# Optimization experiments

Hardware: AMD Instinct MI355X
Metric: run time of the kernel (lower is better)

Reference implementation:

```python
import jax, jax.numpy as jnp
import numpy as np


def setup_inputs() -> dict:
    key = jax.random.key(0)
    ks = jax.random.split(key, 7)
    C, Cq = 128, 16  # channels, channels//8
    B, H, W = 8, 64, 64
    s = 0.05
    return {
        "x": jax.random.normal(ks[0], (B, C, H, W), jnp.float32),
        "wq": jax.random.normal(ks[1], (Cq, C), jnp.float32) * s,
        "bq": jnp.zeros((Cq,), jnp.float32),
        "wk": jax.random.normal(ks[2], (Cq, C), jnp.float32) * s,
        "bk": jnp.zeros((Cq,), jnp.float32),
        "wv": jax.random.normal(ks[3], (C, C), jnp.float32) * s,
        "bv": jnp.zeros((C,), jnp.float32),
    }


def reference(x, wq, bq, wk, bk, wv, bv):
    B, C, H, W = x.shape
    N = H * W
    dk = wq.shape[0]  # channels // 8
    xf = x.reshape(B, C, N)  # [B, C, N]
    # 1x1 convs == per-pixel linear maps over channels
    q = jnp.einsum('oc,bcn->bon', wq, xf) + bq[None, :, None]  # [B, dk, N]
    k = jnp.einsum('oc,bcn->bon', wk, xf) + bk[None, :, None]  # [B, dk, N]
    v = jnp.einsum('oc,bcn->bon', wv, xf) + bv[None, :, None]  # [B, C, N]
    # scores[b,i,j] = <q[:,i], k[:,j]> / sqrt(dk)
    scores = jnp.einsum('bdi,bdj->bij', q, k) / jnp.sqrt(jnp.asarray(dk, x.dtype))
    attn = jax.nn.softmax(scores, axis=-1)  # softmax over key dim j
    # out[b,c,i] = sum_j v[b,c,j] * attn[b,i,j]
    out = jnp.einsum('bcj,bij->bci', v, attn)
    return out.reshape(B, C, H, W) + x
```

## Files before the change

kernel.cpp:

```cpp
#include <hip/hip_runtime.h>
#include <hip/hip_bf16.h>

#define BATCH 8
#define CDIM  128
#define DK    16
#define NPIX  4096
#define VSTR  72

typedef __attribute__((ext_vector_type(4)))  float    f32x4;
typedef __attribute__((ext_vector_type(16))) float    f32x16;
typedef __attribute__((ext_vector_type(8)))  short    s16x8;
typedef __attribute__((ext_vector_type(4)))  unsigned u32x4;

__device__ __forceinline__ short f2bf(float f) {
    union { float fv; unsigned u; } un; un.fv = f;
    unsigned r = un.u + 0x7FFFu + ((un.u >> 16) & 1u);
    return (short)(r >> 16);
}
__device__ __forceinline__ float bf2f(short s) {
    union { unsigned u; float f; } un; un.u = ((unsigned)(unsigned short)s) << 16;
    return un.f;
}
__device__ __forceinline__ float fexp2(float x) {
#if __has_builtin(__builtin_amdgcn_exp2f)
    return __builtin_amdgcn_exp2f(x);
#else
    return exp2f(x);
#endif
}
__device__ __forceinline__ unsigned pkbf(float lo, float hi) {
    __hip_bfloat162 h = __float22bfloat162_rn(make_float2(lo, hi));
    return *reinterpret_cast<unsigned*>(&h);
}
__device__ __forceinline__ f32x16 zero16() {
    f32x16 z;
    #pragma unroll
    for (int i = 0; i < 16; ++i) z[i] = 0.f;
    return z;
}

#define C2F 0.36067376022224085f
#define WPFRAGS (10 * 4 * 64)

__global__ __launch_bounds__(256) void wprep(
    const float* __restrict__ wq, const float* __restrict__ wk,
    const float* __restrict__ wv, short* __restrict__ Wp)
{
    const int mt   = blockIdx.x;
    const int t    = threadIdx.x;
    const int kt   = t >> 6;
    const int lane = t & 63;
    const int m    = mt * 16 + (lane & 15);
    const int c0   = kt * 32 + ((lane >> 4) << 3);

    const float* src; float scl = 1.f;
    if (m < 16)      { src = wq + m * CDIM; scl = C2F; }
    else if (m < 32) { src = wk + (m - 16) * CDIM; }
    else             { src = wv + (m - 32) * CDIM; }

    s16x8 frag;
    #pragma unroll
    for (int i = 0; i < 8; ++i) frag[i] = f2bf(src[c0 + i] * scl);
    *(s16x8*)(Wp + (((size_t)(mt * 4 + kt) * 64 + lane) << 3)) = frag;
}

__global__ __launch_bounds__(256) void qkv_proj(
    const float* __restrict__ x, const short* __restrict__ Wp,
    const float* __restrict__ bq, const float* __restrict__ bk,
    const float* __restrict__ bv,
    short* __restrict__ Qt, short* __restrict__ Kt, short* __restrict__ Vb)
{
    const int tid   = threadIdx.x;
    const int bid   = blockIdx.x;
    const int b     = bid >> 6;
    const int nbase = (bid & 63) << 6;

    const int lane = tid & 63;
    const int lo   = lane & 15;
    const int hi   = lane >> 4;
    const int n    = ((tid >> 6) << 4) + lo;
    const int ng   = nbase + n;

    const float* xb = x + (((size_t)(b * CDIM)) << 12) + ng;

    s16x8 bfr[4];
    #pragma unroll
    for (int kt = 0; kt < 4; ++kt) {
        const float* xp = xb + (((size_t)(kt * 32 + hi * 8)) << 12);
        float v0 = xp[0];
        float v1 = xp[(size_t)1 << 12];
        float v2 = xp[(size_t)2 << 12];
        float v3 = xp[(size_t)3 << 12];
        float v4 = xp[(size_t)4 << 12];
        float v5 = xp[(size_t)5 << 12];
        float v6 = xp[(size_t)6 << 12];
        float v7 = xp[(size_t)7 << 12];
        union { u32x4 u; s16x8 v; } pk;
        pk.u[0] = pkbf(v0, v1); pk.u[1] = pkbf(v2, v3);
        pk.u[2] = pkbf(v4, v5); pk.u[3] = pkbf(v6, v7);
        bfr[kt] = pk.v;
    }

    f32x4 acc[10];
    #pragma unroll
    for (int mt = 0; mt < 10; ++mt) { acc[mt][0]=0.f; acc[mt][1]=0.f; acc[mt][2]=0.f; acc[mt][3]=0.f; }

    #pragma unroll
    for (int kt = 0; kt < 4; ++kt) {
        #pragma unroll
        for (int mt = 0; mt < 10; ++mt) {
            const s16x8 af = *(const s16x8*)(Wp + (((size_t)(mt * 4 + kt) * 64 + lane) << 3));
            acc[mt] = __builtin_amdgcn_mfma_f32_16x16x32_bf16(af, bfr[kt], acc[mt], 0, 0, 0);
        }
    }

    const int m4 = hi << 2;
    {
        uint2 pk;
        pk.x = pkbf(acc[0][0] + bq[m4 + 0] * C2F, acc[0][1] + bq[m4 + 1] * C2F);
        pk.y = pkbf(acc[0][2] + bq[m4 + 2] * C2F, acc[0][3] + bq[m4 + 3] * C2F);
        *(uint2*)(Qt + ((((size_t)(b << 12)) + ng) << 4) + m4) = pk;
    }
    {
        uint2 pk;
        pk.x = pkbf(acc[1][0] + bk[m4 + 0], acc[1][1] + bk[m4 + 1]);
        pk.y = pkbf(acc[1][2] + bk[m4 + 2], acc[1][3] + bk[m4 + 3]);
        *(uint2*)(Kt + ((((size_t)(b << 12)) + ng) << 4) + m4) = pk;
    }
    #pragma unroll
    for (int mt = 2; mt < 10; ++mt) {
        #pragma unroll
        for (int r = 0; r < 4; ++r) {
            const int c = (mt - 2) * 16 + m4 + r;
            Vb[(((size_t)(b * CDIM + c)) << 12) + ng] = f2bf(acc[mt][r] + bv[c]);
        }
    }
}

template<int KSPLIT, bool DIRECT>
__global__ __launch_bounds__(256, 3) void attn_part(
    const short* __restrict__ Qt, const short* __restrict__ Kt,
    const short* __restrict__ Vb, const float* __restrict__ x,
    float* __restrict__ out, short* __restrict__ Op, float* __restrict__ lsum)
{
    constexpr int NKEY = NPIX / KSPLIT;
    constexpr int NT   = NKEY / 64;
    __shared__ __align__(16) short vs[2][CDIM * VSTR];

    const int tid = threadIdx.x;
    const int bid = blockIdx.x;
    const int qb  = bid & 31;
    const int kc  = (bid >> 5) % KSPLIT;
    const int b   = bid / (32 * KSPLIT);
    const int q0  = qb * 128 + (tid >> 6) * 32;
    const int l31 = tid & 31;
    const int hi2 = (tid >> 5) & 1;
    const int kq  = hi2 << 3;
    const int pi  = (l31 & ~12) | ((l31 & 4) << 1) | ((l31 & 8) >> 1);

    const s16x8 qB = *(const s16x8*)(Qt + (((size_t)(b << 12) + q0 + l31) << 4) + kq);

    const int j8  = tid & 7;
    const int cb8 = tid >> 3;
    const short* vsrc = Vb + (((size_t)(b * CDIM + cb8)) << 12) + (j8 << 3);
    const int vdoff = cb8 * VSTR + (j8 << 3);
    const size_t cstr = (size_t)32 << 12;

    const int jbase0 = kc * NKEY;
    const short* ktb = Kt + ((size_t)(b << 12) << 4);

    f32x16 O0 = zero16(), O1 = zero16(), O2 = zero16(), O3 = zero16();
    float l_acc = 0.f;

    s16x8 r0, r1, r2, r3;
    #define VLOAD(jb) do {                                   \
        r0 = *(const s16x8*)(vsrc + (jb));                   \
        r1 = *(const s16x8*)(vsrc + (jb) + cstr);            \
        r2 = *(const s16x8*)(vsrc + (jb) + 2 * cstr);        \
        r3 = *(const s16x8*)(vsrc + (jb) + 3 * cstr);        \
    } while (0)
    #define VSTORE(bufi) do {                                \
        short* vd_ = &vs[bufi][vdoff];                       \
        *(s16x8*)(vd_)             = r0;                     \
        *(s16x8*)(vd_ + 32 * VSTR) = r1;                     \
        *(s16x8*)(vd_ + 64 * VSTR) = r2;                     \
        *(s16x8*)(vd_ + 96 * VSTR) = r3;                     \
    } while (0)
    #define KLOAD(jb) (*(const s16x8*)(ktb + (((size_t)((jb) + pi)) << 4) + kq))
    #define LDSV(vb_, ct, ch) (*(const s16x8*)((vb_) + ((ct) * 32 + l31) * VSTR + ((ch) << 3)))

    #define LOADVF(dst, h, vb_) do {                         \
        const int ch_ = ((h) << 1) | hi2;                    \
        dst[0] = LDSV(vb_, 0, ch_);                          \
        dst[1] = LDSV(vb_, 1, ch_);                          \
        dst[2] = LDSV(vb_, 2, ch_);                          \
        dst[3] = LDSV(vb_, 3, ch_);                          \
    } while (0)

    #define HALFP(sv, ktl, vf) do {                                             \
        float p0 = fexp2(sv[8*(ktl)+0]), p1 = fexp2(sv[8*(ktl)+1]);            \
        float p2 = fexp2(sv[8*(ktl)+2]), p3 = fexp2(sv[8*(ktl)+3]);            \
        float p4 = fexp2(sv[8*(ktl)+4]), p5 = fexp2(sv[8*(ktl)+5]);            \
        float p6 = fexp2(sv[8*(ktl)+6]), p7 = fexp2(sv[8*(ktl)+7]);            \
        l_acc += ((p0+p1)+(p2+p3)) + ((p4+p5)+(p6+p7));                        \
        union { u32x4 u; s16x8 v; } pc_;                                       \
        pc_.u[0] = pkbf(p0,p1); pc_.u[1] = pkbf(p2,p3);                        \
        pc_.u[2] = pkbf(p4,p5); pc_.u[3] = pkbf(p6,p7);                        \
        O0 = __builtin_amdgcn_mfma_f32_32x32x16_bf16(vf[0], pc_.v, O0, 0,0,0); \
        O1 = __builtin_amdgcn_mfma_f32_32x32x16_bf16(vf[1], pc_.v, O1, 0,0,0); \
        O2 = __builtin_amdgcn_mfma_f32_32x32x16_bf16(vf[2], pc_.v, O2, 0,0,0); \
        O3 = __builtin_amdgcn_mfma_f32_32x32x16_bf16(vf[3], pc_.v, O3, 0,0,0); \
    } while (0)

    VLOAD(jbase0);
    s16x8 kA0c = KLOAD(jbase0);
    s16x8 kA1c = KLOAD(jbase0 + 32);
    VSTORE(0);
    __syncthreads();

    for (int t = 0; t < NT; ++t) {
        const int jb  = jbase0 + (t << 6);
        const int cur = t & 1;
        const short* vcur = &vs[cur][0];

        s16x8 vfA[4], vfB[4];
        LOADVF(vfA, 0, vcur);

        s16x8 kA0n, kA1n;
        if (t + 1 < NT) {
            VLOAD(jb + 64);
            kA0n = KLOAD(jb + 64);
            kA1n = KLOAD(jb + 96);
        }

        f32x16 s0 = __builtin_amdgcn_mfma_f32_32x32x16_bf16(kA0c, qB, zero16(), 0, 0, 0);
        LOADVF(vfB, 1, vcur);
        HALFP(s0, 0, vfA);
        LOADVF(vfA, 2, vcur);
        HALFP(s0, 1, vfB);
        f32x16 s1 = __builtin_amdgcn_mfma_f32_32x32x16_bf16(kA1c, qB, zero16(), 0, 0, 0);
        LOADVF(vfB, 3, vcur);
        HALFP(s1, 0, vfA);
        HALFP(s1, 1, vfB);

        if (t + 1 < NT) {
            VSTORE(cur ^ 1);
            kA0c = kA0n; kA1c = kA1n;
        }
        __syncthreads();
    }

    float l_tot = l_acc + __shfl_xor(l_acc, 32);
    const int ncol = q0 + l31;

    if constexpr (DIRECT) {
        const float inv = 1.f / l_tot;
        #define EPID(Ov, ct) do {                                              \
            _Pragma("unroll")                                                  \
            for (int r = 0; r < 16; ++r) {                                     \
                const int c = (ct)*32 + (r&3) + 8*(r>>2) + (hi2<<2);           \
                const size_t off = (((size_t)(b * CDIM + c)) << 12) + ncol;    \
                out[off] = Ov[r] * inv + x[off];                               \
            } } while (0)
        EPID(O0, 0); EPID(O1, 1); EPID(O2, 2); EPID(O3, 3);
    } else {
        const int prow = (kc * 8 + b) * CDIM;
        #define EPIP(Ov, ct) do {                                              \
            _Pragma("unroll")                                                  \
            for (int r = 0; r < 16; ++r) {                                     \
                const int c = (ct)*32 + (r&3) + 8*(r>>2) + (hi2<<2);           \
                Op[(((size_t)(prow + c)) << 12) + ncol] = f2bf(Ov[r]);         \
            } } while (0)
        EPIP(O0, 0); EPIP(O1, 1); EPIP(O2, 2); EPIP(O3, 3);
        if (!hi2) lsum[(((size_t)(kc * 8 + b)) << 12) + ncol] = l_tot;
    }
}

template<int KSPLIT>
__global__ __launch_bounds__(256) void attn_combine(
    const short* __restrict__ Op, const float* __restrict__ lsum,
    const float* __restrict__ x, float* __restrict__ out)
{
    __shared__ float linv[256];
    const int tid = threadIdx.x;
    const int bid = blockIdx.x;
    const int b   = bid >> 7;
    const int nb  = (bid >> 3) & 15;
    const int cb  = bid & 7;
    const int nbase = nb << 8;

    {
        float s = 0.f;
        #pragma unroll
        for (int k = 0; k < KSPLIT; ++k)
            s += lsum[(((size_t)(k * 8 + b)) << 12) + nbase + tid];
        linv[tid] = 1.f / s;
    }
    __syncthreads();

    const int n8 = (tid & 31) << 3;
    #pragma unroll
    for (int pass = 0; pass < 2; ++pass) {
        const int c = (cb << 4) + (pass << 3) + (tid >> 5);
        const size_t gbase = (((size_t)(b * CDIM + c)) << 12) + nbase + n8;
        float acc[8];
        #pragma unroll
        for (int j = 0; j < 8; ++j) acc[j] = 0.f;
        #pragma unroll
        for (int k = 0; k < KSPLIT; ++k) {
            s16x8 v = *(const s16x8*)(Op + (((size_t)((k * 8 + b) * CDIM + c)) << 12) + nbase + n8);
            #pragma unroll
            for (int j = 0; j < 8; ++j) acc[j] += bf2f(v[j]);
        }
        float4 li0 = *(const float4*)&linv[n8];
        float4 li1 = *(const float4*)&linv[n8 + 4];
        float4 x0  = *(const float4*)(x + gbase);
        float4 x1  = *(const float4*)(x + gbase + 4);
        float4 o0, o1;
        o0.x = acc[0] * li0.x + x0.x;  o0.y = acc[1] * li0.y + x0.y;
        o0.z = acc[2] * li0.z + x0.z;  o0.w = acc[3] * li0.w + x0.w;
        o1.x = acc[4] * li1.x + x1.x;  o1.y = acc[5] * li1.y + x1.y;
        o1.z = acc[6] * li1.z + x1.z;  o1.w = acc[7] * li1.w + x1.w;
        *(float4*)(out + gbase)     = o0;
        *(float4*)(out + gbase + 4) = o1;
    }
}

extern "C" void kernel_launch(void* const* d_in, const int* in_sizes, int n_in,
                              void* d_out, int out_size, void* d_ws, size_t ws_size,
                              hipStream_t stream) {
    const float* x  = (const float*)d_in[0];
    const float* wq = (const float*)d_in[1];
    const float* bq = (const float*)d_in[2];
    const float* wk = (const float*)d_in[3];
    const float* bk = (const float*)d_in[4];
    const float* wv = (const float*)d_in[5];
    const float* bv = (const float*)d_in[6];
    float* out = (float*)d_out;

    short* Qt = (short*)d_ws;
    short* Kt = Qt + (size_t)BATCH * NPIX * DK;
    short* Vw = Kt + (size_t)BATCH * NPIX * DK;
    short* Wpk = Vw + (size_t)BATCH * CDIM * NPIX;
    char*  extra = (char*)(Wpk + (size_t)WPFRAGS * 8);
    const size_t used    = (size_t)(extra - (char*)d_ws);
    const size_t opBytes = (size_t)BATCH * CDIM * NPIX * sizeof(short);
    const size_t lBytes  = (size_t)BATCH * NPIX * sizeof(float);

    wprep<<<dim3(10), dim3(256), 0, stream>>>(wq, wk, wv, Wpk);
    qkv_proj<<<dim3(512), dim3(256), 0, stream>>>(x, Wpk, bq, bk, bv, Qt, Kt, Vw);

    if (used + 4 * (opBytes + lBytes) <= ws_size) {
        short* Opw = (short*)extra;
        float* ls  = (float*)(extra + 4 * opBytes);
        attn_part<4, false><<<dim3(8 * 32 * 4), dim3(256), 0, stream>>>(Qt, Kt, Vw, x, out, Opw, ls);
        attn_combine<4><<<dim3(1024), dim3(256), 0, stream>>>(Opw, ls, x, out);
    } else if (used + 2 * (opBytes + lBytes) <= ws_size) {
        short* Opw = (short*)extra;
        float* ls  = (float*)(extra + 2 * opBytes);
        attn_part<2, false><<<dim3(8 * 32 * 2), dim3(256), 0, stream>>>(Qt, Kt, Vw, x, out, Opw, ls);
        attn_combine<2><<<dim3(1024), dim3(256), 0, stream>>>(Opw, ls, x, out);
    } else {
        attn_part<1, true><<<dim3(8 * 32), dim3(256), 0, stream>>>(Qt, Kt, Vw, x, out, nullptr, nullptr);
    }
}
```

Baseline: 79.36 us.

## Process two query tiles per block to reuse staged V and K tiles

New measurement: 70.76 us. -10.8%, faster.

```diff
diff --git a/kernel.cpp b/kernel.cpp
--- a/kernel.cpp
+++ b/kernel.cpp
@@ -138,7 +138,7 @@
 }
 
 template<int KSPLIT, bool DIRECT>
-__global__ __launch_bounds__(256, 3) void attn_part(
+__global__ __launch_bounds__(256, 2) void attn_part(
     const short* __restrict__ Qt, const short* __restrict__ Kt,
     const short* __restrict__ Vb, const float* __restrict__ x,
     float* __restrict__ out, short* __restrict__ Op, float* __restrict__ lsum)
@@ -149,16 +149,18 @@
 
     const int tid = threadIdx.x;
     const int bid = blockIdx.x;
-    const int qb  = bid & 31;
-    const int kc  = (bid >> 5) % KSPLIT;
-    const int b   = bid / (32 * KSPLIT);
-    const int q0  = qb * 128 + (tid >> 6) * 32;
+    const int qb  = bid & 15;
+    const int kc  = (bid >> 4) % KSPLIT;
+    const int b   = bid / (16 * KSPLIT);
+    const int q0A = qb * 256 + (tid >> 6) * 32;
+    const int q0B = q0A + 128;
     const int l31 = tid & 31;
     const int hi2 = (tid >> 5) & 1;
     const int kq  = hi2 << 3;
     const int pi  = (l31 & ~12) | ((l31 & 4) << 1) | ((l31 & 8) >> 1);
 
-    const s16x8 qB = *(const s16x8*)(Qt + (((size_t)(b << 12) + q0 + l31) << 4) + kq);
+    const s16x8 qBA = *(const s16x8*)(Qt + (((size_t)(b << 12) + q0A + l31) << 4) + kq);
+    const s16x8 qBB = *(const s16x8*)(Qt + (((size_t)(b << 12) + q0B + l31) << 4) + kq);
 
     const int j8  = tid & 7;
     const int cb8 = tid >> 3;
@@ -169,8 +171,9 @@
     const int jbase0 = kc * NKEY;
     const short* ktb = Kt + ((size_t)(b << 12) << 4);
 
-    f32x16 O0 = zero16(), O1 = zero16(), O2 = zero16(), O3 = zero16();
-    float l_acc = 0.f;
+    f32x16 OA0 = zero16(), OA1 = zero16(), OA2 = zero16(), OA3 = zero16();
+    f32x16 OB0 = zero16(), OB1 = zero16(), OB2 = zero16(), OB3 = zero16();
+    float l_accA = 0.f, l_accB = 0.f;
 
     s16x8 r0, r1, r2, r3;
     #define VLOAD(jb) do {                                   \
@@ -188,7 +191,6 @@
     } while (0)
     #define KLOAD(jb) (*(const s16x8*)(ktb + (((size_t)((jb) + pi)) << 4) + kq))
     #define LDSV(vb_, ct, ch) (*(const s16x8*)((vb_) + ((ct) * 32 + l31) * VSTR + ((ch) << 3)))
-
     #define LOADVF(dst, h, vb_) do {                         \
         const int ch_ = ((h) << 1) | hi2;                    \
         dst[0] = LDSV(vb_, 0, ch_);                          \
@@ -197,20 +199,22 @@
         dst[3] = LDSV(vb_, 3, ch_);                          \
     } while (0)
 
-    #define HALFP(sv, ktl, vf) do {                                             \
+    #define HALFP(sv, ktl, vf, Oa, Ob, Oc, Od, lac) do {                        \
         float p0 = fexp2(sv[8*(ktl)+0]), p1 = fexp2(sv[8*(ktl)+1]);            \
         float p2 = fexp2(sv[8*(ktl)+2]), p3 = fexp2(sv[8*(ktl)+3]);            \
         float p4 = fexp2(sv[8*(ktl)+4]), p5 = fexp2(sv[8*(ktl)+5]);            \
         float p6 = fexp2(sv[8*(ktl)+6]), p7 = fexp2(sv[8*(ktl)+7]);            \
-        l_acc += ((p0+p1)+(p2+p3)) + ((p4+p5)+(p6+p7));                        \
+        lac += ((p0+p1)+(p2+p3)) + ((p4+p5)+(p6+p7));                          \
         union { u32x4 u; s16x8 v; } pc_;                                       \
         pc_.u[0] = pkbf(p0,p1); pc_.u[1] = pkbf(p2,p3);                        \
         pc_.u[2] = pkbf(p4,p5); pc_.u[3] = pkbf(p6,p7);                        \
-        O0 = __builtin_amdgcn_mfma_f32_32x32x16_bf16(vf[0], pc_.v, O0, 0,0,0); \
-        O1 = __builtin_amdgcn_mfma_f32_32x32x16_bf16(vf[1], pc_.v, O1, 0,0,0); \
-        O2 = __builtin_amdgcn_mfma_f32_32x32x16_bf16(vf[2], pc_.v, O2, 0,0,0); \
-        O3 = __builtin_amdgcn_mfma_f32_32x32x16_bf16(vf[3], pc_.v, O3, 0,0,0); \
+        Oa = __builtin_amdgcn_mfma_f32_32x32x16_bf16(vf[0], pc_.v, Oa, 0,0,0); \
+        Ob = __builtin_amdgcn_mfma_f32_32x32x16_bf16(vf[1], pc_.v, Ob, 0,0,0); \
+        Oc = __builtin_amdgcn_mfma_f32_32x32x16_bf16(vf[2], pc_.v, Oc, 0,0,0); \
+        Od = __builtin_amdgcn_mfma_f32_32x32x16_bf16(vf[3], pc_.v, Od, 0,0,0); \
     } while (0)
+    #define HALF_A(sv, ktl, vf) HALFP(sv, ktl, vf, OA0, OA1, OA2, OA3, l_accA)
+    #define HALF_B(sv, ktl, vf) HALFP(sv, ktl, vf, OB0, OB1, OB2, OB3, l_accB)
 
     VLOAD(jbase0);
     s16x8 kA0c = KLOAD(jbase0);
@@ -226,53 +230,69 @@
         s16x8 vfA[4], vfB[4];
         LOADVF(vfA, 0, vcur);
 
-        s16x8 kA0n, kA1n;
+        f32x16 s0a = __builtin_amdgcn_mfma_f32_32x32x16_bf16(kA0c, qBA, zero16(), 0, 0, 0);
+        f32x16 s0b = __builtin_amdgcn_mfma_f32_32x32x16_bf16(kA0c, qBB, zero16(), 0, 0, 0);
+
+        if (t + 1 < NT) VLOAD(jb + 64);
+
+        LOADVF(vfB, 1, vcur);
+        HALF_A(s0a, 0, vfA);
+        HALF_B(s0b, 0, vfA);
+        LOADVF(vfA, 2, vcur);
+        HALF_A(s0a, 1, vfB);
+        HALF_B(s0b, 1, vfB);
+
+        f32x16 s1a = __builtin_amdgcn_mfma_f32_32x32x16_bf16(kA1c, qBA, zero16(), 0, 0, 0);
+        f32x16 s1b = __builtin_amdgcn_mfma_f32_32x32x16_bf16(kA1c, qBB, zero16(), 0, 0, 0);
         if (t + 1 < NT) {
-            VLOAD(jb + 64);
-            kA0n = KLOAD(jb + 64);
-            kA1n = KLOAD(jb + 96);
-        }
-
-        f32x16 s0 = __builtin_amdgcn_mfma_f32_32x32x16_bf16(kA0c, qB, zero16(), 0, 0, 0);
-        LOADVF(vfB, 1, vcur);
-        HALFP(s0, 0, vfA);
-        LOADVF(vfA, 2, vcur);
-        HALFP(s0, 1, vfB);
-        f32x16 s1 = __builtin_amdgcn_mfma_f32_32x32x16_bf16(kA1c, qB, zero16(), 0, 0, 0);
+            kA0c = KLOAD(jb + 64);
+            kA1c = KLOAD(jb + 96);
+        }
         LOADVF(vfB, 3, vcur);
-        HALFP(s1, 0, vfA);
-        HALFP(s1, 1, vfB);
-
-        if (t + 1 < NT) {
-            VSTORE(cur ^ 1);
-            kA0c = kA0n; kA1c = kA1n;
-        }
+        HALF_A(s1a, 0, vfA);
+        HALF_B(s1b, 0, vfA);
+        HALF_A(s1a, 1, vfB);
+        HALF_B(s1b, 1, vfB);
+
+        if (t + 1 < NT) VSTORE(cur ^ 1);
         __syncthreads();
     }
 
-    float l_tot = l_acc + __shfl_xor(l_acc, 32);
-    const int ncol = q0 + l31;
+    float l_totA = l_accA + __shfl_xor(l_accA, 32);
+    float l_totB = l_accB + __shfl_xor(l_accB, 32);
+    const int ncolA = q0A + l31;
+    const int ncolB = q0B + l31;
 
     if constexpr (DIRECT) {
-        const float inv = 1.f / l_tot;
-        #define EPID(Ov, ct) do {                                              \
+        const float invA = 1.f / l_totA;
+        const float invB = 1.f / l_totB;
+        #define EPID(Ov, ct, ncol, inv) do {                                   \
             _Pragma("unroll")                                                  \
             for (int r = 0; r < 16; ++r) {                                     \
                 const int c = (ct)*32 + (r&3) + 8*(r>>2) + (hi2<<2);           \
-                const size_t off = (((size_t)(b * CDIM + c)) << 12) + ncol;    \
-                out[off] = Ov[r] * inv + x[off];                               \
+                const size_t off = (((size_t)(b * CDIM + c)) << 12) + (ncol);  \
+                out[off] = Ov[r] * (inv) + x[off];                             \
             } } while (0)
-        EPID(O0, 0); EPID(O1, 1); EPID(O2, 2); EPID(O3, 3);
+        EPID(OA0, 0, ncolA, invA); EPID(OA1, 1, ncolA, invA);
+        EPID(OA2, 2, ncolA, invA); EPID(OA3, 3, ncolA, invA);
+        EPID(OB0, 0, ncolB, invB); EPID(OB1, 1, ncolB, invB);
+        EPID(OB2, 2, ncolB, invB); EPID(OB3, 3, ncolB, invB);
     } else {
         const int prow = (kc * 8 + b) * CDIM;
-        #define EPIP(Ov, ct) do {                                              \
+        #define EPIP(Ov, ct, ncol) do {                                        \
             _Pragma("unroll")                                                  \
             for (int r = 0; r < 16; ++r) {                                     \
                 const int c = (ct)*32 + (r&3) + 8*(r>>2) + (hi2<<2);           \
-                Op[(((size_t)(prow + c)) << 12) + ncol] = f2bf(Ov[r]);         \
+                Op[(((size_t)(prow + c)) << 12) + (ncol)] = f2bf(Ov[r]);       \
             } } while (0)
-        EPIP(O0, 0); EPIP(O1, 1); EPIP(O2, 2); EPIP(O3, 3);
-        if (!hi2) lsum[(((size_t)(kc * 8 + b)) << 12) + ncol] = l_tot;
+        EPIP(OA0, 0, ncolA); EPIP(OA1, 1, ncolA);
+        EPIP(OA2, 2, ncolA); EPIP(OA3, 3, ncolA);
+        EPIP(OB0, 0, ncolB); EPIP(OB1, 1, ncolB);
+        EPIP(OB2, 2, ncolB); EPIP(OB3, 3, ncolB);
+        if (!hi2) {
+            lsum[(((size_t)(kc * 8 + b)) << 12) + ncolA] = l_totA;
+            lsum[(((size_t)(kc * 8 + b)) << 12) + ncolB] = l_totB;
+        }
     }
 }
 
@@ -353,14 +373,14 @@
     if (used + 4 * (opBytes + lBytes) <= ws_size) {
         short* Opw = (short*)extra;
         float* ls  = (float*)(extra + 4 * opBytes);
-        attn_part<4, false><<<dim3(8 * 32 * 4), dim3(256), 0, stream>>>(Qt, Kt, Vw, x, out, Opw, ls);
+        attn_part<4, false><<<dim3(8 * 16 * 4), dim3(256), 0, stream>>>(Qt, Kt, Vw, x, out, Opw, ls);
         attn_combine<4><<<dim3(1024), dim3(256), 0, stream>>>(Opw, ls, x, out);
     } else if (used + 2 * (opBytes + lBytes) <= ws_size) {
         short* Opw = (short*)extra;
         float* ls  = (float*)(extra + 2 * opBytes);
-        attn_part<2, false><<<dim3(8 * 32 * 2), dim3(256), 0, stream>>>(Qt, Kt, Vw, x, out, Opw, ls);
+        attn_part<2, false><<<dim3(8 * 16 * 2), dim3(256), 0, stream>>>(Qt, Kt, Vw, x, out, Opw, ls);
         attn_combine<2><<<dim3(1024), dim3(256), 0, stream>>>(Opw, ls, x, out);
     } else {
-        attn_part<1, true><<<dim3(8 * 32), dim3(256), 0, stream>>>(Qt, Kt, Vw, x, out, nullptr, nullptr);
-    }
-}
+        attn_part<1, true><<<dim3(8 * 16), dim3(256), 0, stream>>>(Qt, Kt, Vw, x, out, nullptr, nullptr);
+    }
+}
```
